# Kernel optimization log

Hardware: AMD Instinct MI355X
Metric: run time of the kernel (lower is better)

## Reference

```python
import jax, jax.numpy as jnp
import numpy as np

L2_REG = 0.25

def setup_inputs() -> dict:
    key = jax.random.key(0)
    k0, k1, k2, k3 = jax.random.split(key, 4)
    B, D, A, K = 16384, 128, 8192, 64
    image_embed = jax.random.normal(k0, (B, D), dtype=jnp.float32)
    anc_ind = jax.random.randint(k1, (A,), 0, B, dtype=jnp.int64)
    pos_ind = jax.random.randint(k2, (A,), 0, B, dtype=jnp.int64)
    neg_ind = jax.random.randint(k3, (A, K), 0, B, dtype=jnp.int64)
    return {"image_embed": image_embed, "anc_ind": anc_ind,
            "pos_ind": pos_ind, "neg_ind": neg_ind}

def reference(image_embed, anc_ind, pos_ind, neg_ind):
    # Gather anchor/positive/negative embeddings
    a = image_embed[anc_ind]          # [A, D]
    p = image_embed[pos_ind]          # [A, D]
    n = image_embed[neg_ind]          # [A, K, D]
    # inner[i, k] = a_i . (n_ik - p_i)
    inner = jnp.einsum('ad,akd->ak', a, n - p[:, None, :])  # [A, K]
    # log(1 + sum_k exp(inner)) computed stably via logaddexp(0, logsumexp)
    per_anchor = jnp.logaddexp(jnp.float32(0.0), jax.nn.logsumexp(inner, axis=1))
    npair = jnp.mean(per_anchor)
    # l2 term: mean L2 norm of all batch embeddings, added once per anchor / len -> once
    l2 = L2_REG * jnp.mean(jnp.linalg.norm(image_embed, axis=1))
    return npair + l2
```

## Files before the change

kernel.cpp:

```cpp
#include <hip/hip_runtime.h>
#include <hip/hip_bf16.h>
#include <math.h>

#define B_SZ 16384
#define D_DIM 128
#define A_SZ 8192
#define K_SZ 64
#define L2_REG_F 0.25f
#define CONV_BLK 512
#define NBLK 2048

__device__ __forceinline__ float wave_reduce_sum(float v) {
    #pragma unroll
    for (int off = 32; off > 0; off >>= 1)
        v += __shfl_xor(v, off, 64);
    return v;
}

__device__ __forceinline__ float wave_reduce_max(float v) {
    #pragma unroll
    for (int off = 32; off > 0; off >>= 1)
        v = fmaxf(v, __shfl_xor(v, off, 64));
    return v;
}

__device__ __forceinline__ float blo(unsigned u) { return __uint_as_float(u << 16); }
__device__ __forceinline__ float bhi(unsigned u) { return __uint_as_float(u & 0xFFFF0000u); }

__global__ __launch_bounds__(256) void convert_kernel(const float* __restrict__ embed,
                                                      unsigned* __restrict__ tab,
                                                      float* __restrict__ partial) {
    __shared__ float red[4];
    const int wave = threadIdx.x >> 6;
    const int lane = threadIdx.x & 63;
    const int gw   = blockIdx.x * 4 + wave;
    float acc = 0.f;
    #pragma unroll
    for (int r = 0; r < B_SZ / (CONV_BLK * 4); ++r) {
        const int row = gw * (B_SZ / (CONV_BLK * 4)) + r;
        const float2* rr = (const float2*)(embed + (size_t)row * D_DIM);
        float2 v = rr[lane];
        acc += sqrtf(wave_reduce_sum(v.x * v.x + v.y * v.y));
        __hip_bfloat16 bx = __float2bfloat16(v.x);
        __hip_bfloat16 by = __float2bfloat16(v.y);
        tab[(size_t)row * 64 + lane] = ((unsigned)__bfloat16_as_ushort(by) << 16)
                                     | (unsigned)__bfloat16_as_ushort(bx);
    }
    if (lane == 0) red[wave] = acc * (L2_REG_F / (float)B_SZ);
    __syncthreads();
    if (threadIdx.x == 0)
        partial[blockIdx.x] = red[0] + red[1] + red[2] + red[3];
}

__global__ __launch_bounds__(256) void npair_kernel(const unsigned* __restrict__ tab,
                                                    const int* __restrict__ anc_ind,
                                                    const int* __restrict__ pos_ind,
                                                    const int* __restrict__ neg_ind,
                                                    float* __restrict__ partial) {
    __shared__ __align__(16) float a_lds[4][D_DIM];
    __shared__ float red[4];
    const int wave = threadIdx.x >> 6;
    const int lane = threadIdx.x & 63;
    const int i    = blockIdx.x * 4 + wave;

    const int ai = anc_ind[i];
    const int pi = pos_ind[i];
    const int ni = neg_ind[(size_t)i * K_SZ + lane];

    unsigned ua = tab[(size_t)ai * 64 + lane];
    unsigned up = tab[(size_t)pi * 64 + lane];
    float ax = blo(ua), ay = bhi(ua);
    a_lds[wave][2 * lane]     = ax;
    a_lds[wave][2 * lane + 1] = ay;
    float ap = wave_reduce_sum(ax * blo(up) + ay * bhi(up));

    const uint4*  nr = (const uint4*)(tab + (size_t)ni * 64);
    const float4* al = (const float4*)a_lds[wave];
    float s0 = 0.f, s1 = 0.f;
    #pragma unroll
    for (int j = 0; j < 16; j += 4) {
        uint4 q0 = nr[j], q1 = nr[j + 1], q2 = nr[j + 2], q3 = nr[j + 3];
        float4 a0 = al[2 * j + 0], a1 = al[2 * j + 1];
        float4 a2 = al[2 * j + 2], a3 = al[2 * j + 3];
        float4 a4 = al[2 * j + 4], a5 = al[2 * j + 5];
        float4 a6 = al[2 * j + 6], a7 = al[2 * j + 7];
        s0 += a0.x * blo(q0.x) + a0.y * bhi(q0.x) + a0.z * blo(q0.y) + a0.w * bhi(q0.y);
        s1 += a1.x * blo(q0.z) + a1.y * bhi(q0.z) + a1.z * blo(q0.w) + a1.w * bhi(q0.w);
        s0 += a2.x * blo(q1.x) + a2.y * bhi(q1.x) + a2.z * blo(q1.y) + a2.w * bhi(q1.y);
        s1 += a3.x * blo(q1.z) + a3.y * bhi(q1.z) + a3.z * blo(q1.w) + a3.w * bhi(q1.w);
        s0 += a4.x * blo(q2.x) + a4.y * bhi(q2.x) + a4.z * blo(q2.y) + a4.w * bhi(q2.y);
        s1 += a5.x * blo(q2.z) + a5.y * bhi(q2.z) + a5.z * blo(q2.w) + a5.w * bhi(q2.w);
        s0 += a6.x * blo(q3.x) + a6.y * bhi(q3.x) + a6.z * blo(q3.y) + a6.w * bhi(q3.y);
        s1 += a7.x * blo(q3.z) + a7.y * bhi(q3.z) + a7.z * blo(q3.w) + a7.w * bhi(q3.w);
    }
    float inner = (s0 + s1) - ap;

    float m  = wave_reduce_max(inner);
    float se = wave_reduce_sum(__expf(inner - m));
    float lse = m + __logf(se);
    float per = (lse > 0.f) ? lse + log1pf(__expf(-lse)) : log1pf(__expf(lse));

    if (lane == 0) red[wave] = per * (1.0f / (float)A_SZ);
    __syncthreads();
    if (threadIdx.x == 0)
        partial[blockIdx.x] = red[0] + red[1] + red[2] + red[3];
}

__global__ __launch_bounds__(256) void f32_kernel(const float* __restrict__ embed,
                                                  const int* __restrict__ anc_ind,
                                                  const int* __restrict__ pos_ind,
                                                  const int* __restrict__ neg_ind,
                                                  float* __restrict__ partial) {
    __shared__ __align__(16) float a_lds[4][D_DIM];
    __shared__ float red[4];
    const int wave = threadIdx.x >> 6;
    const int lane = threadIdx.x & 63;
    const int gw   = blockIdx.x * 4 + wave;

    float acc_l2 = 0.f;
    #pragma unroll
    for (int r = 0; r < 2; ++r) {
        const int row = gw * 2 + r;
        const float2* rr = (const float2*)(embed + (size_t)row * D_DIM);
        float2 v = rr[lane];
        acc_l2 += sqrtf(wave_reduce_sum(v.x * v.x + v.y * v.y));
    }
    const int i  = gw;
    const int ai = anc_ind[i];
    const int pi = pos_ind[i];
    const int ni = neg_ind[(size_t)i * K_SZ + lane];
    const float2* ar = (const float2*)(embed + (size_t)ai * D_DIM);
    const float2* pr = (const float2*)(embed + (size_t)pi * D_DIM);
    float2 a2 = ar[lane];
    float2 p2 = pr[lane];
    a_lds[wave][2 * lane]     = a2.x;
    a_lds[wave][2 * lane + 1] = a2.y;
    float ap = wave_reduce_sum(a2.x * p2.x + a2.y * p2.y);
    const float4* nr = (const float4*)(embed + (size_t)ni * D_DIM);
    const float4* al = (const float4*)a_lds[wave];
    float s0 = 0.f, s1 = 0.f, s2 = 0.f, s3 = 0.f;
    #pragma unroll
    for (int j = 0; j < D_DIM / 4; j += 4) {
        float4 n0 = nr[j], n1 = nr[j + 1], n2 = nr[j + 2], n3 = nr[j + 3];
        float4 a0 = al[j], a1 = al[j + 1], a2v = al[j + 2], a3 = al[j + 3];
        s0 += a0.x * n0.x + a0.y * n0.y + a0.z * n0.z + a0.w * n0.w;
        s1 += a1.x * n1.x + a1.y * n1.y + a1.z * n1.z + a1.w * n1.w;
        s2 += a2v.x * n2.x + a2v.y * n2.y + a2v.z * n2.z + a2v.w * n2.w;
        s3 += a3.x * n3.x + a3.y * n3.y + a3.z * n3.z + a3.w * n3.w;
    }
    float inner = (s0 + s1) + (s2 + s3) - ap;
    float m  = wave_reduce_max(inner);
    float se = wave_reduce_sum(__expf(inner - m));
    float lse = m + __logf(se);
    float per = (lse > 0.f) ? lse + log1pf(__expf(-lse)) : log1pf(__expf(lse));
    float combined = per * (1.0f / (float)A_SZ) + acc_l2 * (L2_REG_F / (float)B_SZ);
    if (lane == 0) red[wave] = combined;
    __syncthreads();
    if (threadIdx.x == 0)
        partial[blockIdx.x] = red[0] + red[1] + red[2] + red[3];
}

__global__ __launch_bounds__(256) void finalize_kernel(const float* __restrict__ partial,
                                                       int n, float* __restrict__ out) {
    __shared__ float red[4];
    const int wave = threadIdx.x >> 6;
    const int lane = threadIdx.x & 63;
    float v = 0.f;
    for (int j = threadIdx.x; j < n; j += 256) v += partial[j];
    v = wave_reduce_sum(v);
    if (lane == 0) red[wave] = v;
    __syncthreads();
    if (threadIdx.x == 0)
        out[0] = red[0] + red[1] + red[2] + red[3];
}

extern "C" void kernel_launch(void* const* d_in, const int* in_sizes, int n_in,
                              void* d_out, int out_size, void* d_ws, size_t ws_size,
                              hipStream_t stream) {
    const float* embed = (const float*)d_in[0];
    const int*   anc   = (const int*)d_in[1];
    const int*   pos   = (const int*)d_in[2];
    const int*   neg   = (const int*)d_in[3];
    float* out = (float*)d_out;

    const size_t tab_bytes = (size_t)B_SZ * (D_DIM / 2) * sizeof(unsigned);
    const size_t need = tab_bytes + (CONV_BLK + NBLK) * sizeof(float);

    if (ws_size >= need) {
        unsigned* tab     = (unsigned*)d_ws;
        float*    partial = (float*)((char*)d_ws + tab_bytes);
        convert_kernel<<<CONV_BLK, 256, 0, stream>>>(embed, tab, partial);
        npair_kernel<<<NBLK, 256, 0, stream>>>(tab, anc, pos, neg, partial + CONV_BLK);
        finalize_kernel<<<1, 256, 0, stream>>>(partial, CONV_BLK + NBLK, out);
    } else {
        float* partial = (float*)d_ws;
        f32_kernel<<<NBLK, 256, 0, stream>>>(embed, anc, pos, neg, partial);
        finalize_kernel<<<1, 256, 0, stream>>>(partial, NBLK, out);
    }
}
```

Baseline: 92.97 us.

## Split each negative row across four lanes for more coalesced gathers

The negative-embedding gather is restructured so that each group of four lanes cooperatively loads one 256-byte bf16 row. Previously each lane read a whole row by itself. Each lane now reads a 16-byte chunk, and partial dot products are combined with cross-lane shuffles over four passes. This is meant to turn strided per-lane row reads into contiguous segments per memory instruction. The cost is extra shuffle and select instructions, with the anchor LDS reads indexed differently per lane group.

```diff
diff --git a/kernel.cpp b/kernel.cpp
--- a/kernel.cpp
+++ b/kernel.cpp
@@ -65,7 +65,7 @@
 
     const int ai = anc_ind[i];
     const int pi = pos_ind[i];
-    const int ni = neg_ind[(size_t)i * K_SZ + lane];
+    const int nid_all = neg_ind[(size_t)i * K_SZ + lane];
 
     unsigned ua = tab[(size_t)ai * 64 + lane];
     unsigned up = tab[(size_t)pi * 64 + lane];
@@ -74,26 +74,29 @@
     a_lds[wave][2 * lane + 1] = ay;
     float ap = wave_reduce_sum(ax * blo(up) + ay * bhi(up));
 
-    const uint4*  nr = (const uint4*)(tab + (size_t)ni * 64);
     const float4* al = (const float4*)a_lds[wave];
-    float s0 = 0.f, s1 = 0.f;
-    #pragma unroll
-    for (int j = 0; j < 16; j += 4) {
-        uint4 q0 = nr[j], q1 = nr[j + 1], q2 = nr[j + 2], q3 = nr[j + 3];
-        float4 a0 = al[2 * j + 0], a1 = al[2 * j + 1];
-        float4 a2 = al[2 * j + 2], a3 = al[2 * j + 3];
-        float4 a4 = al[2 * j + 4], a5 = al[2 * j + 5];
-        float4 a6 = al[2 * j + 6], a7 = al[2 * j + 7];
-        s0 += a0.x * blo(q0.x) + a0.y * bhi(q0.x) + a0.z * blo(q0.y) + a0.w * bhi(q0.y);
-        s1 += a1.x * blo(q0.z) + a1.y * bhi(q0.z) + a1.z * blo(q0.w) + a1.w * bhi(q0.w);
-        s0 += a2.x * blo(q1.x) + a2.y * bhi(q1.x) + a2.z * blo(q1.y) + a2.w * bhi(q1.y);
-        s1 += a3.x * blo(q1.z) + a3.y * bhi(q1.z) + a3.z * blo(q1.w) + a3.w * bhi(q1.w);
-        s0 += a4.x * blo(q2.x) + a4.y * bhi(q2.x) + a4.z * blo(q2.y) + a4.w * bhi(q2.y);
-        s1 += a5.x * blo(q2.z) + a5.y * bhi(q2.z) + a5.z * blo(q2.w) + a5.w * bhi(q2.w);
-        s0 += a6.x * blo(q3.x) + a6.y * bhi(q3.x) + a6.z * blo(q3.y) + a6.w * bhi(q3.y);
-        s1 += a7.x * blo(q3.z) + a7.y * bhi(q3.z) + a7.z * blo(q3.w) + a7.w * bhi(q3.w);
-    }
-    float inner = (s0 + s1) - ap;
+    const int r = lane & 15;
+    const int c = lane >> 4;
+
+    float inner = 0.f;
+    #pragma unroll
+    for (int p = 0; p < 4; ++p) {
+        const int nidx = __shfl(nid_all, p * 16 + r, 64);
+        const uint4* nb = (const uint4*)(tab + (size_t)nidx * 64);
+        float s = 0.f;
+        #pragma unroll
+        for (int j = 0; j < 4; ++j) {
+            const int u = j * 4 + c;
+            uint4 q = nb[u];
+            float4 a0 = al[2 * u], a1 = al[2 * u + 1];
+            s += a0.x * blo(q.x) + a0.y * bhi(q.x) + a0.z * blo(q.y) + a0.w * bhi(q.y);
+            s += a1.x * blo(q.z) + a1.y * bhi(q.z) + a1.z * blo(q.w) + a1.w * bhi(q.w);
+        }
+        s += __shfl_xor(s, 16, 64);
+        s += __shfl_xor(s, 32, 64);
+        if (c == p) inner = s;
+    }
+    inner -= ap;
 
     float m  = wave_reduce_max(inner);
     float se = wave_reduce_sum(__expf(inner - m));
```

After: 89.46 us. 3.8% less time.
